# Kernel optimization log

Measured on AMD Instinct MI355X. Metric: run time of the kernel, lower is better.

Reference implementation:

```python
import jax, jax.numpy as jnp
import numpy as np

DIM = 1024
HEADS = 8
DIM_HEAD = 64
INNER = HEADS * DIM_HEAD  # 512
N_PATCHES = 256
SCALE = DIM_HEAD ** -0.5


def setup_inputs() -> dict:
    key = jax.random.key(0)
    ks = jax.random.split(key, 6)
    s = lambda fan_in: 1.0 / np.sqrt(fan_in)
    return {
        "x": jax.random.normal(ks[0], (64, N_PATCHES, DIM), dtype=jnp.float32),
        "Wq": jax.random.normal(ks[1], (DIM, INNER), dtype=jnp.float32) * s(DIM),
        "Wkv": jax.random.normal(ks[2], (DIM, 2 * INNER), dtype=jnp.float32) * s(DIM),
        "Wout": jax.random.normal(ks[3], (INNER, DIM), dtype=jnp.float32) * s(INNER),
        "bout": jax.random.normal(ks[4], (DIM,), dtype=jnp.float32) * 0.01,
        "Wspec": jax.random.normal(ks[5], (N_PATCHES, 3 * N_PATCHES), dtype=jnp.float32) * s(N_PATCHES),
    }


def reference(x, Wq, Wkv, Wout, bout, Wspec):
    b, n, d = x.shape
    # ---- spatial: single center-query attention ----
    x_center = x[:, n // 2, :]                      # [b, d]
    q = (x_center @ Wq).reshape(b, HEADS, DIM_HEAD)  # [b, h, dh]
    kv = x @ Wkv                                     # [b, n, 2*inner]
    k, v = jnp.split(kv, 2, axis=-1)
    k = k.reshape(b, n, HEADS, DIM_HEAD).transpose(0, 2, 1, 3)  # [b, h, n, dh]
    v = v.reshape(b, n, HEADS, DIM_HEAD).transpose(0, 2, 1, 3)
    logits = jnp.einsum('bhd,bhnd->bhn', q, k) * SCALE
    attn = jax.nn.softmax(logits, axis=-1)           # [b, h, n]
    out = jnp.einsum('bhn,bhnd->bhd', attn, v).reshape(b, INNER)
    # torch expands attn over n identical rows BEFORE to_out; the rows are
    # identical, so broadcasting the projected row is the same math.
    spatial = out @ Wout + bout                      # [b, d]
    spatial_out = jnp.broadcast_to(spatial[:, None, :], (b, n, d))
    # ---- spectral: attention over transposed (feature) axis ----
    x_t = x.transpose(0, 2, 1)                       # [b, d, n]
    qkv = x_t @ Wspec                                # [b, d, 3n]
    q_s, k_s, v_s = jnp.split(qkv, 3, axis=-1)       # v_s unused (as in source)
    spec_logits = jnp.einsum('bin,bjn->bij', q_s, k_s) * SCALE  # [b, d, d]
    spec_weights = jax.nn.softmax(spec_logits, axis=-1)
    return jnp.einsum('bnd,bde->bne', spatial_out, spec_weights)
```

## Files before the change

kernel.cpp:

```cpp
#include <hip/hip_runtime.h>
#include <hip/hip_bf16.h>
#include <cstdint>

typedef _Float16 f16;
typedef _Float16 half8 __attribute__((ext_vector_type(8)));
typedef float f32x4 __attribute__((ext_vector_type(4)));

#define SCALE 0.125f

#define GLL(src, dst) __builtin_amdgcn_global_load_lds( \
    (const __attribute__((address_space(1))) unsigned int*)(src), \
    (__attribute__((address_space(3))) unsigned int*)(dst), 16, 0, 0)

__global__ __launch_bounds__(256) void prep_xT(const float* __restrict__ x, f16* __restrict__ xT) {
  __shared__ f16 tile[64][34];
  int dt = blockIdx.x, nt = blockIdx.y, b = blockIdx.z;
  int t = threadIdx.x;
#pragma unroll
  for (int p = 0; p < 2; ++p) {
    int n = p*32 + (t >> 3), dg = t & 7;
    f32x4 v = *(const f32x4*)(x + ((size_t)b*256 + nt*64 + n)*1024 + dt*32 + dg*4);
    f16* dst = &tile[n][dg*4];
    dst[0] = (f16)v[0]; dst[1] = (f16)v[1]; dst[2] = (f16)v[2]; dst[3] = (f16)v[3];
  }
  __syncthreads();
  {
    int d = t >> 3, ng = t & 7;
    half8 o;
#pragma unroll
    for (int j = 0; j < 8; ++j) o[j] = tile[ng*8 + j][d];
    *(half8*)(xT + ((size_t)b*1024 + dt*32 + d)*256 + nt*64 + ng*8) = o;
  }
}

__global__ __launch_bounds__(256) void prep_Wspec16(const float* __restrict__ W, f16* __restrict__ Wt) {
  int row = blockIdx.x, t = threadIdx.x;
  Wt[(size_t)row*512 + t]       = (f16)W[(size_t)row*768 + t];
  Wt[(size_t)row*512 + 256 + t] = (f16)W[(size_t)row*768 + 256 + t];
}

template<int KSTEPS, int AST, int BST, int CST, bool SCALEQ>
__global__ __launch_bounds__(256) void gemm128(const f16* __restrict__ Ag, const f16* __restrict__ Bg,
                                               f16* __restrict__ Cg, size_t aB, size_t bB, size_t cB) {
  __shared__ f16 As[2][128*32];
  __shared__ f16 Bs[2][128*32];
  const f16* A = Ag + (size_t)blockIdx.z*aB;
  const f16* B = Bg + (size_t)blockIdx.z*bB;
  f16* C = Cg + (size_t)blockIdx.z*cB;
  int t = threadIdx.x, lane = t & 63, wave = t >> 6;
  int l15 = lane & 15, l4 = lane >> 4;
  int wm = wave & 1, wn = wave >> 1;
  size_t m0 = (size_t)blockIdx.x*128, n0 = (size_t)blockIdx.y*128;
  f32x4 acc[4][4];
#pragma unroll
  for (int i=0;i<4;++i)
#pragma unroll
    for (int j=0;j<4;++j) acc[i][j] = (f32x4){0.f,0.f,0.f,0.f};
  int rowS[2], chS[2];
#pragma unroll
  for (int c=0;c<2;++c) {
    int slot = c*256 + t;
    rowS[c] = slot >> 2;
    chS[c]  = (slot & 3) ^ ((slot >> 3) & 3);
  }
  int pc = (l4 ^ ((l15 >> 1) & 3)) * 8;

  auto STAGE = [&](int buf, int ks) {
    int k0 = ks*32;
#pragma unroll
    for (int c=0;c<2;++c) {
      GLL(A + (m0 + rowS[c])*(size_t)AST + k0 + chS[c]*8, &As[buf][(c*256 + wave*64)*8]);
      GLL(B + (n0 + rowS[c])*(size_t)BST + k0 + chS[c]*8, &Bs[buf][(c*256 + wave*64)*8]);
    }
  };

  STAGE(0, 0);
#pragma unroll 2
  for (int ks = 0; ks < KSTEPS; ++ks) {
    int cur = ks & 1;
    if (ks + 1 < KSTEPS) {
      STAGE(cur ^ 1, ks + 1);
      asm volatile("s_waitcnt vmcnt(4)" ::: "memory");
    } else {
      asm volatile("s_waitcnt vmcnt(0)" ::: "memory");
    }
    __builtin_amdgcn_s_barrier();
    __builtin_amdgcn_sched_barrier(0);
    half8 a[4], bb[4];
    const f16* Af = &As[cur][(wm*64 + l15)*32 + pc];
    const f16* Bf = &Bs[cur][(wn*64 + l15)*32 + pc];
#pragma unroll
    for (int mi=0;mi<4;++mi) a[mi]  = *(const half8*)(Af + mi*16*32);
#pragma unroll
    for (int ni=0;ni<4;++ni) bb[ni] = *(const half8*)(Bf + ni*16*32);
    __builtin_amdgcn_s_setprio(1);
#pragma unroll
    for (int mi=0;mi<4;++mi)
#pragma unroll
      for (int ni=0;ni<4;++ni)
        acc[mi][ni] = __builtin_amdgcn_mfma_f32_16x16x32_f16(a[mi], bb[ni], acc[mi][ni], 0,0,0);
    __builtin_amdgcn_s_setprio(0);
    __builtin_amdgcn_sched_barrier(0);
    __builtin_amdgcn_s_barrier();
  }
  float cscale = SCALEQ ? SCALE : 1.0f;
#pragma unroll
  for (int mi=0;mi<4;++mi)
#pragma unroll
    for (int ni=0;ni<4;++ni)
#pragma unroll
      for (int j=0;j<4;++j) {
        size_t row = m0 + wm*64 + mi*16 + 4*l4 + j;
        size_t col = n0 + wn*64 + ni*16 + l15;
        C[row*CST + col] = (f16)(acc[mi][ni][j] * cscale);
      }
}

__global__ __launch_bounds__(256) void qk(const float* __restrict__ x, const float* __restrict__ Wq,
                                          float* __restrict__ qbuf, float* __restrict__ attnout) {
  int b = blockIdx.x, h = blockIdx.y;
  int t = threadIdx.x;
  __shared__ float xc[1024];
  __shared__ float part[4][64];
  if (t < 64) attnout[(size_t)b*512 + h*64 + t] = 0.f;
  const float* xcg = x + ((size_t)b*256 + 128)*1024;
#pragma unroll
  for (int i = 0; i < 4; ++i) xc[t + 256*i] = xcg[t + 256*i];
  __syncthreads();
  int d = t & 63, chunk = t >> 6;
  float s = 0.f;
  const float* wq = Wq + (size_t)(chunk*256)*512 + h*64 + d;
#pragma unroll 8
  for (int c = 0; c < 256; ++c) s += xc[chunk*256 + c] * wq[(size_t)c*512];
  part[chunk][d] = s;
  __syncthreads();
  if (t < 64) qbuf[(size_t)b*512 + h*64 + t] = part[0][t]+part[1][t]+part[2][t]+part[3][t];
}

__global__ __launch_bounds__(256) void uk(const float* __restrict__ Wkv, const float* __restrict__ qbuf,
                                          f16* __restrict__ u16) {
  int h = blockIdx.x, dc = blockIdx.y;
  int t = threadIdx.x;
  __shared__ float Wk[32][64];
  __shared__ float qT[64][65];
  {
    int j = t & 63, g = t >> 6;
#pragma unroll
    for (int rr = 0; rr < 8; ++rr) {
      int dd = g*8 + rr;
      Wk[dd][j] = Wkv[(size_t)(dc*32 + dd)*1024 + h*64 + j];
    }
#pragma unroll
    for (int rr = 0; rr < 16; ++rr) {
      int bb = g*16 + rr;
      qT[j][bb] = qbuf[(size_t)bb*512 + h*64 + j];
    }
  }
  __syncthreads();
  int b = t & 63, dq = t >> 6;
#pragma unroll
  for (int i = 0; i < 8; ++i) {
    int dd = dq*8 + i;
    float s = 0.f;
#pragma unroll 8
    for (int j = 0; j < 64; ++j) s += qT[j][b] * Wk[dd][j];
    u16[((size_t)b*16 + h)*1024 + dc*32 + dd]       = (f16)s;
    u16[((size_t)b*16 + 8 + h)*1024 + dc*32 + dd]   = (f16)0.f;
  }
}

__global__ __launch_bounds__(64) void lgk(const float* __restrict__ x, const f16* __restrict__ u16,
                                          float* __restrict__ logitbuf) {
  int mt = blockIdx.x, b = blockIdx.y;
  int lane = threadIdx.x, l15 = lane & 15, l4 = lane >> 4;
  const float* Ap = x + ((size_t)b*256 + mt*16 + l15)*1024 + 8*l4;
  const f16* Bp = u16 + ((size_t)b*16 + l15)*1024 + 8*l4;
  f32x4 acc = (f32x4){0.f,0.f,0.f,0.f};
#pragma unroll 8
  for (int ks = 0; ks < 32; ++ks) {
    f32x4 lo = *(const f32x4*)(Ap + ks*32);
    f32x4 hi = *(const f32x4*)(Ap + ks*32 + 4);
    half8 h;
    h[0]=(f16)lo[0]; h[1]=(f16)lo[1]; h[2]=(f16)lo[2]; h[3]=(f16)lo[3];
    h[4]=(f16)hi[0]; h[5]=(f16)hi[1]; h[6]=(f16)hi[2]; h[7]=(f16)hi[3];
    acc = __builtin_amdgcn_mfma_f32_16x16x32_f16(h, *(const half8*)(Bp + ks*32), acc, 0,0,0);
  }
  if (l15 < 8) {
#pragma unroll
    for (int j = 0; j < 4; ++j)
      logitbuf[((size_t)b*256 + mt*16 + 4*l4 + j)*8 + l15] = acc[j];
  }
}

__global__ __launch_bounds__(64) void xbk(const float* __restrict__ logitbuf, const f16* __restrict__ xT,
                                          f16* __restrict__ xbar) {
  int dt = blockIdx.x, b = blockIdx.y;
  int lane = threadIdx.x, l15 = lane & 15, l4 = lane >> 4;
  const float* lp = logitbuf + (size_t)b*256*8;
  float Z = 0.f;
  if (l15 < 8) {
#pragma unroll 8
    for (int n = l4*64; n < l4*64 + 64; ++n)
      Z += __expf(lp[(size_t)n*8 + l15] * SCALE);
  }
  Z += __shfl_xor(Z, 16);
  Z += __shfl_xor(Z, 32);
  float rZ = (l15 < 8) ? (1.0f / Z) : 0.f;
  const f16* Bp = xT + ((size_t)b*1024 + dt*16 + l15)*256 + 8*l4;
  f32x4 acc = (f32x4){0.f,0.f,0.f,0.f};
#pragma unroll
  for (int ks = 0; ks < 8; ++ks) {
    half8 a;
    if (l15 < 8) {
#pragma unroll
      for (int j = 0; j < 8; ++j) {
        int n = ks*32 + l4*8 + j;
        a[j] = (f16)(__expf(lp[(size_t)n*8 + l15] * SCALE) * rZ);
      }
    } else {
#pragma unroll
      for (int j = 0; j < 8; ++j) a[j] = (f16)0.f;
    }
    acc = __builtin_amdgcn_mfma_f32_16x16x32_f16(a, *(const half8*)(Bp + ks*32), acc, 0,0,0);
  }
  if (l4 < 2) {
#pragma unroll
    for (int j = 0; j < 4; ++j)
      xbar[((size_t)b*8 + 4*l4 + j)*1024 + dt*16 + l15] = (f16)acc[j];
  }
}

__global__ __launch_bounds__(256) void vk(const f16* __restrict__ xbar, const float* __restrict__ Wkv,
                                          float* __restrict__ attnout) {
  int h = blockIdx.x, dc = blockIdx.y, bc = blockIdx.z;
  int t = threadIdx.x;
  __shared__ float Wv[256][64];
  {
    int j = t & 63, g = t >> 6;
#pragma unroll
    for (int rr = 0; rr < 64; ++rr) {
      int dd = g*64 + rr;
      Wv[dd][j] = Wkv[(size_t)(dc*256 + dd)*1024 + 512 + h*64 + j];
    }
  }
  __syncthreads();
  int j = t & 63, bq = t >> 6;
  float s[4] = {0.f,0.f,0.f,0.f};
  const f16* xp[4];
#pragma unroll
  for (int bl = 0; bl < 4; ++bl)
    xp[bl] = xbar + ((size_t)(bc*16 + bq*4 + bl)*8 + h)*1024 + dc*256;
  for (int d8 = 0; d8 < 32; ++d8) {
    half8 xv[4];
#pragma unroll
    for (int bl = 0; bl < 4; ++bl) xv[bl] = *(const half8*)(xp[bl] + d8*8);
#pragma unroll
    for (int i = 0; i < 8; ++i) {
      float w = Wv[d8*8 + i][j];
#pragma unroll
      for (int bl = 0; bl < 4; ++bl) s[bl] += (float)xv[bl][i] * w;
    }
  }
#pragma unroll
  for (int bl = 0; bl < 4; ++bl)
    atomicAdd(&attnout[(size_t)(bc*16 + bq*4 + bl)*512 + h*64 + j], s[bl]);
}

__global__ __launch_bounds__(256) void spatialf(const float* __restrict__ attnout, const float* __restrict__ Wout,
                                                const float* __restrict__ bout, float* __restrict__ spatial,
                                                float* __restrict__ rvec) {
  int ec = blockIdx.x, b = blockIdx.y;
  int t = threadIdx.x;
  __shared__ float ao[512];
  rvec[(size_t)b*1024 + ec*256 + t] = 0.f;
  ao[t]       = attnout[(size_t)b*512 + t];
  ao[t + 256] = attnout[(size_t)b*512 + 256 + t];
  __syncthreads();
  int e = ec*256 + t;
  float a0 = bout[e], a1 = 0.f;
#pragma unroll 8
  for (int i = 0; i < 512; i += 2) {
    a0 += ao[i]     * Wout[(size_t)i*1024 + e];
    a1 += ao[i + 1] * Wout[(size_t)(i + 1)*1024 + e];
  }
  spatial[(size_t)b*1024 + e] = a0 + a1;
}

__global__ __launch_bounds__(1024, 4) void speck(const f16* __restrict__ Y, const f16* __restrict__ xT,
                                                 const float* __restrict__ spatial, float* __restrict__ r) {
  __shared__ __attribute__((aligned(16))) char smem[163840];
  f16* As = (f16*)smem;
  f16* Bs = (f16*)(smem + 32768);
  float* sz   = (float*)smem;
  float* zfin = (float*)(smem + 4096);
  int bid = blockIdx.x;
  int xcd = bid & 7, q = bid >> 3;
  int b = xcd*8 + (q >> 4);
  int iblk = q & 15;
  int t = threadIdx.x, lane = t & 63, wave = t >> 6;
  int l15 = lane & 15, l4 = lane >> 4;
  const f16* Yb  = Y  + (size_t)b*262144;
  const f16* xTb = xT + (size_t)b*262144;
  int i0 = iblk*64;

  f32x4 acc[4][4];
#pragma unroll
  for (int mi=0;mi<4;++mi)
#pragma unroll
    for (int ni=0;ni<4;++ni) acc[mi][ni] = (f32x4){0.f,0.f,0.f,0.f};
  int pc = (l4 ^ ((l15 >> 1) & 3)) * 8;

#pragma unroll
  for (int g = 0; g < 2; ++g) {
    int u = (wave*2 + g)*64 + lane;
    int rA = u >> 5, v = u & 31;
    int s = v ^ (rA & 7);
    GLL(Yb + (size_t)(i0 + rA)*256 + (s >> 2)*32 + (s & 3)*8, As + ((wave*2 + g)*64)*8);
  }
  auto STAGE_B = [&](int slot, int ks) {
    int k0 = ks*32;
#pragma unroll
    for (int c = 0; c < 4; ++c) {
      int u2 = c*64 + lane;
      int row = u2 >> 2, pchk = u2 & 3;
      int ch = pchk ^ (((row & 15) >> 1) & 3);
      GLL(xTb + (size_t)(wave*64 + row)*256 + k0 + ch*8,
          Bs + ((wave*2 + slot)*256 + c*64)*8);
    }
  };
  STAGE_B(0, 0);
  STAGE_B(1, 1);
  asm volatile("s_waitcnt vmcnt(8)" ::: "memory");
  __builtin_amdgcn_s_barrier();

  int axor = l15 & 7;
#pragma unroll
  for (int ks = 0; ks < 8; ++ks) {
    int slot = ks & 1;
    if (ks < 7) asm volatile("s_waitcnt vmcnt(4)" ::: "memory");
    else        asm volatile("s_waitcnt vmcnt(0)" ::: "memory");
    __builtin_amdgcn_sched_barrier(0);
    half8 a[4], bb[4];
    const f16* Bbase = Bs + (wave*2 + slot)*2048;
    int physA = ((ks*4 + l4) ^ axor)*8;
#pragma unroll
    for (int mi = 0; mi < 4; ++mi) a[mi]  = *(const half8*)(As + (mi*16 + l15)*256 + physA);
#pragma unroll
    for (int ni = 0; ni < 4; ++ni) bb[ni] = *(const half8*)(Bbase + (ni*16 + l15)*32 + pc);
    asm volatile("s_waitcnt lgkmcnt(0)" ::: "memory");
    __builtin_amdgcn_sched_barrier(0);
    if (ks < 6) STAGE_B(slot, ks + 2);
    __builtin_amdgcn_s_setprio(1);
#pragma unroll
    for (int ni = 0; ni < 4; ++ni)
#pragma unroll
      for (int mi = 0; mi < 4; ++mi)
        acc[mi][ni] = __builtin_amdgcn_mfma_f32_16x16x32_f16(a[mi], bb[ni], acc[mi][ni], 0,0,0);
    __builtin_amdgcn_s_setprio(0);
    __builtin_amdgcn_sched_barrier(0);
  }
  float zr[4][4];
#pragma unroll
  for (int mi=0;mi<4;++mi)
#pragma unroll
    for (int jj=0;jj<4;++jj) {
      float s = 0.f;
#pragma unroll
      for (int ni=0;ni<4;++ni) {
        float e = __expf(acc[mi][ni][jj]);
        acc[mi][ni][jj] = e;
        s += e;
      }
#pragma unroll
      for (int o=1;o<16;o<<=1) s += __shfl_xor(s, o);
      zr[mi][jj] = s;
    }
  __syncthreads();
  if (l15 == 0) {
#pragma unroll
    for (int mi=0;mi<4;++mi)
#pragma unroll
      for (int jj=0;jj<4;++jj) sz[(mi*16 + 4*l4 + jj)*16 + wave] = zr[mi][jj];
  }
  __syncthreads();
  {
    float v = sz[t];
#pragma unroll
    for (int o=1;o<16;o<<=1) v += __shfl_xor(v, o);
    if ((t & 15) == 0) zfin[t >> 4] = v;
  }
  __syncthreads();
  float f[4][4];
#pragma unroll
  for (int mi=0;mi<4;++mi)
#pragma unroll
    for (int jj=0;jj<4;++jj) {
      int row = mi*16 + 4*l4 + jj;
      f[mi][jj] = spatial[(size_t)b*1024 + i0 + row] / zfin[row];
    }
  float* rb = r + (size_t)b*1024;
#pragma unroll
  for (int ni=0;ni<4;++ni) {
    float v = 0.f;
#pragma unroll
    for (int mi=0;mi<4;++mi)
#pragma unroll
      for (int jj=0;jj<4;++jj) v += f[mi][jj]*acc[mi][ni][jj];
    v += __shfl_xor(v, 16);
    v += __shfl_xor(v, 32);
    if (l4 == 0) atomicAdd(rb + wave*64 + ni*16 + l15, v);
  }
}

__global__ __launch_bounds__(256) void bcast(const float* __restrict__ r, float* __restrict__ out) {
  size_t row = blockIdx.x;
  int b = (int)(row >> 8);
  f32x4 v = *(const f32x4*)(r + (size_t)b*1024 + threadIdx.x*4);
  *(f32x4*)(out + row*1024 + (size_t)threadIdx.x*4) = v;
}

extern "C" void kernel_launch(void* const* d_in, const int* in_sizes, int n_in,
                              void* d_out, int out_size, void* d_ws, size_t ws_size,
                              hipStream_t stream) {
  const float* x     = (const float*)d_in[0];
  const float* Wq    = (const float*)d_in[1];
  const float* Wkv   = (const float*)d_in[2];
  const float* Wout  = (const float*)d_in[3];
  const float* bout  = (const float*)d_in[4];
  const float* Wspec = (const float*)d_in[5];
  float* out = (float*)d_out;
  char* ws = (char*)d_ws;
  f16*   Ybuf     = (f16*)(ws);
  f16*   u16pad   = (f16*)(ws);
  float* logitbuf = (float*)(ws + 2097152);
  f16*   xbar     = (f16*)(ws + 3145728);
  float* qbuf     = (float*)(ws + 5242880);
  f16*   MT       = (f16*)(ws + 33554432);
  f16*   xT       = (f16*)(ws + 67108864);
  f16*   Wspec16  = (f16*)(ws + 102760448);
  float* attnout  = (float*)(ws + 103022592);
  float* spatial  = (float*)(ws + 103153664);
  float* rvec     = (float*)(ws + 103415808);
  (void)in_sizes; (void)n_in; (void)out_size; (void)ws_size;

  prep_xT     <<<dim3(32, 4, 64), dim3(256), 0, stream>>>(x, xT);
  prep_Wspec16<<<dim3(256),       dim3(256), 0, stream>>>(Wspec, Wspec16);
  gemm128<8,512,512,256,false><<<dim3(2, 2, 1), dim3(256), 0, stream>>>(Wspec16 + 256, Wspec16, MT, 0, 0, 0);
  qk          <<<dim3(64, 8),     dim3(256), 0, stream>>>(x, Wq, qbuf, attnout);
  uk          <<<dim3(8, 32),     dim3(256), 0, stream>>>(Wkv, qbuf, u16pad);
  lgk         <<<dim3(16, 64),    dim3(64),  0, stream>>>(x, u16pad, logitbuf);
  xbk         <<<dim3(64, 64),    dim3(64),  0, stream>>>(logitbuf, xT, xbar);
  vk          <<<dim3(8, 4, 4),   dim3(256), 0, stream>>>(xbar, Wkv, attnout);
  spatialf    <<<dim3(4, 64),     dim3(256), 0, stream>>>(attnout, Wout, bout, spatial, rvec);
  gemm128<8,256,256,256,true><<<dim3(8, 2, 64), dim3(256), 0, stream>>>(xT, MT, Ybuf,
                                                                        262144, 0, 262144);
  speck       <<<dim3(1024),      dim3(1024), 0, stream>>>(Ybuf, xT, spatial, rvec);
  bcast       <<<dim3(16384),     dim3(256), 0, stream>>>(rvec, out);
}
```

Baseline: 210.8 us.

## Fuse Y = xT·MT projection into spectral attention kernel, dropping separate GEMM

The separate gemm128 launch that computed Y = xT·MT into a global buffer is removed. Instead, each speck block loads its 64-row xT tile and the full 256x256 MT into LDS, computes its slice of Y with MFMA, scales it, and writes it back into LDS as the A operand for the main loop. This removes a kernel launch and the global write and read of Y. In exchange, every block redundantly loads MT and does an extra serialized prologue before the main pipeline.

Measured after the change: 201.4 us. 1.05x faster.

```diff
diff --git a/kernel.cpp b/kernel.cpp
--- a/kernel.cpp
+++ b/kernel.cpp
@@ -286,7 +286,7 @@
   spatial[(size_t)b*1024 + e] = a0 + a1;
 }
 
-__global__ __launch_bounds__(1024, 4) void speck(const f16* __restrict__ Y, const f16* __restrict__ xT,
+__global__ __launch_bounds__(1024, 4) void speck(const f16* __restrict__ MT, const f16* __restrict__ xT,
                                                  const float* __restrict__ spatial, float* __restrict__ r) {
   __shared__ __attribute__((aligned(16))) char smem[163840];
   f16* As = (f16*)smem;
@@ -299,24 +299,47 @@
   int iblk = q & 15;
   int t = threadIdx.x, lane = t & 63, wave = t >> 6;
   int l15 = lane & 15, l4 = lane >> 4;
-  const f16* Yb  = Y  + (size_t)b*262144;
   const f16* xTb = xT + (size_t)b*262144;
   int i0 = iblk*64;
-
-  f32x4 acc[4][4];
-#pragma unroll
-  for (int mi=0;mi<4;++mi)
-#pragma unroll
-    for (int ni=0;ni<4;++ni) acc[mi][ni] = (f32x4){0.f,0.f,0.f,0.f};
-  int pc = (l4 ^ ((l15 >> 1) & 3)) * 8;
+  int axor = l15 & 7;
 
 #pragma unroll
   for (int g = 0; g < 2; ++g) {
     int u = (wave*2 + g)*64 + lane;
     int rA = u >> 5, v = u & 31;
     int s = v ^ (rA & 7);
-    GLL(Yb + (size_t)(i0 + rA)*256 + (s >> 2)*32 + (s & 3)*8, As + ((wave*2 + g)*64)*8);
-  }
+    GLL(xTb + (size_t)(i0 + rA)*256 + (s >> 2)*32 + (s & 3)*8, As + ((wave*2 + g)*64)*8);
+  }
+#pragma unroll
+  for (int g = 0; g < 8; ++g) {
+    int ub = g*1024 + wave*64;
+    int u = ub + lane;
+    int row = u >> 5, v = u & 31;
+    int s = v ^ (row & 7);
+    GLL(MT + (size_t)row*256 + (s >> 2)*32 + (s & 3)*8, Bs + ub*8);
+  }
+  asm volatile("s_waitcnt vmcnt(0)" ::: "memory");
+  __builtin_amdgcn_s_barrier();
+  __builtin_amdgcn_sched_barrier(0);
+
+  int r0 = (wave & 3)*16, c0 = (wave >> 2)*64;
+  f32x4 accy[4];
+#pragma unroll
+  for (int ci = 0; ci < 4; ++ci) accy[ci] = (f32x4){0.f,0.f,0.f,0.f};
+#pragma unroll
+  for (int ks = 0; ks < 8; ++ks) {
+    int ls = ks*4 + l4;
+    half8 ax = *(const half8*)(As + (r0 + l15)*256 + ((ls ^ axor)*8));
+#pragma unroll
+    for (int ci = 0; ci < 4; ++ci) {
+      int c = c0 + ci*16 + l15;
+      half8 bmt = *(const half8*)(Bs + c*256 + ((ls ^ (c & 7))*8));
+      accy[ci] = __builtin_amdgcn_mfma_f32_16x16x32_f16(ax, bmt, accy[ci], 0,0,0);
+    }
+  }
+  __builtin_amdgcn_sched_barrier(0);
+  __builtin_amdgcn_s_barrier();
+
   auto STAGE_B = [&](int slot, int ks) {
     int k0 = ks*32;
 #pragma unroll
@@ -330,10 +353,27 @@
   };
   STAGE_B(0, 0);
   STAGE_B(1, 1);
-  asm volatile("s_waitcnt vmcnt(8)" ::: "memory");
+#pragma unroll
+  for (int ci = 0; ci < 4; ++ci) {
+    int col = c0 + ci*16 + l15;
+    int ls2 = col >> 3, off = col & 7;
+#pragma unroll
+    for (int jj = 0; jj < 4; ++jj) {
+      int row = r0 + 4*l4 + jj;
+      As[row*256 + ((ls2 ^ (row & 7))*8) + off] = (f16)(accy[ci][jj] * SCALE);
+    }
+  }
+  asm volatile("s_waitcnt lgkmcnt(0)" ::: "memory");
+  __builtin_amdgcn_sched_barrier(0);
   __builtin_amdgcn_s_barrier();
 
-  int axor = l15 & 7;
+  f32x4 acc[4][4];
+#pragma unroll
+  for (int mi=0;mi<4;++mi)
+#pragma unroll
+    for (int ni=0;ni<4;++ni) acc[mi][ni] = (f32x4){0.f,0.f,0.f,0.f};
+  int pc = (l4 ^ ((l15 >> 1) & 3)) * 8;
+
 #pragma unroll
   for (int ks = 0; ks < 8; ++ks) {
     int slot = ks & 1;
@@ -430,7 +470,6 @@
   const float* Wspec = (const float*)d_in[5];
   float* out = (float*)d_out;
   char* ws = (char*)d_ws;
-  f16*   Ybuf     = (f16*)(ws);
   f16*   u16pad   = (f16*)(ws);
   float* logitbuf = (float*)(ws + 2097152);
   f16*   xbar     = (f16*)(ws + 3145728);
@@ -452,8 +491,6 @@
   xbk         <<<dim3(64, 64),    dim3(64),  0, stream>>>(logitbuf, xT, xbar);
   vk          <<<dim3(8, 4, 4),   dim3(256), 0, stream>>>(xbar, Wkv, attnout);
   spatialf    <<<dim3(4, 64),     dim3(256), 0, stream>>>(attnout, Wout, bout, spatial, rvec);
-  gemm128<8,256,256,256,true><<<dim3(8, 2, 64), dim3(256), 0, stream>>>(xT, MT, Ybuf,
-                                                                        262144, 0, 262144);
-  speck       <<<dim3(1024),      dim3(1024), 0, stream>>>(Ybuf, xT, spatial, rvec);
+  speck       <<<dim3(1024),      dim3(1024), 0, stream>>>(MT, xT, spatial, rvec);
   bcast       <<<dim3(16384),     dim3(256), 0, stream>>>(rvec, out);
 }
```
